# Performance work log

Measured on AMD Instinct MI355X. Metric: run time of the kernel, lower is better.

Reference implementation:

```python
import jax, jax.numpy as jnp
import numpy as np

B = 262144
FEATURES = 16
HID = 24
OUT = 784


def setup_inputs() -> dict:
    key = jax.random.key(0)
    ks = jax.random.split(key, 5)
    return {
        "x": jax.random.normal(ks[0], (B, FEATURES), dtype=jnp.float32),
        "W1": jax.random.normal(ks[1], (FEATURES, HID), dtype=jnp.float32) * 0.1,
        "b1": jax.random.normal(ks[2], (HID,), dtype=jnp.float32) * 0.1,
        "W2": jax.random.normal(ks[3], (HID, OUT), dtype=jnp.float32) * 0.1,
        "b2": jax.random.normal(ks[4], (OUT,), dtype=jnp.float32) * 0.1,
    }


def _relu_approx_sigmoid(x):
    # Original: relu(relu(x @ (0.25*I) + (ones-0.5)) @ (-I) + ones) @ (-I) + ones
    # x @ (0.25*I) == 0.25*x ; ones-0.5 == 0.5 ; y @ (-I) == -y.
    # => 1 - relu(1 - relu(0.25*x + 0.5))  (== clamp(0.25*x+0.5, 0, 1))
    a = jax.nn.relu(0.25 * x + 0.5)
    return 1.0 - jax.nn.relu(1.0 - a)


def reference(x, W1, b1, W2, b2):
    h = jax.nn.relu(x @ W1 + b1)          # [B, 24]
    return _relu_approx_sigmoid(h @ W2 + b2)  # [B, 784]
```

## Files before the change

### kernel.cpp

```cpp
#include <hip/hip_runtime.h>


typedef _Float16 f16x8 __attribute__((ext_vector_type(8)));
typedef float    f32x4 __attribute__((ext_vector_type(4)));
typedef unsigned int u32;

static __device__ __forceinline__ u32 pk_h2(float lo, float hi) {
    return __builtin_bit_cast(u32, __builtin_amdgcn_cvt_pkrtz(lo, hi));
}

#define THREADS 512
#define ROWS 256
#define F 16
#define H 24
#define NOUT 784
#define NCOLT 49
#define KP 12

__launch_bounds__(THREADS, 4)
__global__ void decoder_kernel(const float* __restrict__ x,
                               const float* __restrict__ W1,
                               const float* __restrict__ b1,
                               const float* __restrict__ W2,
                               const float* __restrict__ b2,
                               float* __restrict__ out) {
    __shared__ float w1t[H][F];
    __shared__ float b1s[H];
    __shared__ u32   hbuf[ROWS][16];
    __shared__ u32   w2b[NOUT][16];
    __shared__ float b2s[NOUT];

    const int tid  = threadIdx.x;
    const int row0 = blockIdx.x * ROWS;

    for (int idx = tid; idx < F * H; idx += THREADS) {
        const int i = idx / H, j = idx % H;
        w1t[j][i] = W1[idx];
    }
    if (tid < H) b1s[tid] = b1[tid];

    for (int c = tid; c < NOUT; c += THREADS)
        b2s[c] = fmaf(b2[c], 0.25f, 0.5f);

    for (int item = tid; item < NOUT * KP; item += THREADS) {
        const int col = item / KP, kp = item - col * KP;
        const float a = W2[(2 * kp + 0) * NOUT + col];
        const float c = W2[(2 * kp + 1) * NOUT + col];
        w2b[col][kp] = pk_h2(0.25f * a, 0.25f * c);
    }
    for (int item = tid; item < NOUT * 4; item += THREADS) {
        const int col = item >> 2, kp = 12 + (item & 3);
        w2b[col][kp] = 0u;
    }

    if (tid < ROWS) {
        float4 xv[4];
        const float* xr = x + (size_t)(row0 + tid) * F;
        #pragma unroll
        for (int q = 0; q < 4; ++q)
            xv[q] = *reinterpret_cast<const float4*>(&xr[q * 4]);

        #pragma unroll
        for (int g = 0; g < 3; ++g) {
            float hj[8];
            #pragma unroll
            for (int jj = 0; jj < 8; ++jj) {
                const int j = g * 8 + jj;
                float acc = b1s[j];
                #pragma unroll
                for (int q = 0; q < 4; ++q) {
                    const float4 wv = *reinterpret_cast<const float4*>(&w1t[j][q * 4]);
                    acc = fmaf(xv[q].x, wv.x, acc);
                    acc = fmaf(xv[q].y, wv.y, acc);
                    acc = fmaf(xv[q].z, wv.z, acc);
                    acc = fmaf(xv[q].w, wv.w, acc);
                }
                hj[jj] = fmaxf(acc, 0.0f);
            }
            uint4 p;
            p.x = pk_h2(hj[0], hj[1]);
            p.y = pk_h2(hj[2], hj[3]);
            p.z = pk_h2(hj[4], hj[5]);
            p.w = pk_h2(hj[6], hj[7]);
            *reinterpret_cast<uint4*>(&hbuf[tid][g * 4]) = p;
        }
        *reinterpret_cast<uint4*>(&hbuf[tid][12]) = make_uint4(0u, 0u, 0u, 0u);
    }

    __syncthreads();

    const int wave = tid >> 6;
    const int lane = tid & 63;
    const int lg   = lane >> 4;
    const int lm   = lane & 15;

    const f16x8 a0 = __builtin_bit_cast(f16x8,
        *reinterpret_cast<const uint4*>(&hbuf[wave * 32 + lm][lg * 4]));
    const f16x8 a1 = __builtin_bit_cast(f16x8,
        *reinterpret_cast<const uint4*>(&hbuf[wave * 32 + 16 + lm][lg * 4]));

    float* outp = out + ((size_t)row0 + wave * 32 + lg * 4) * NOUT + lm;

    for (int ct = 0; ct < NCOLT; ++ct) {
        const int cb = ct * 16;
        const f16x8 bf = __builtin_bit_cast(f16x8,
            *reinterpret_cast<const uint4*>(&w2b[cb + lm][lg * 4]));
        const float bb = b2s[cb + lm];
        f32x4 acc0 = {bb, bb, bb, bb};
        f32x4 acc1 = {bb, bb, bb, bb};
        acc0 = __builtin_amdgcn_mfma_f32_16x16x32_f16(a0, bf, acc0, 0, 0, 0);
        acc1 = __builtin_amdgcn_mfma_f32_16x16x32_f16(a1, bf, acc1, 0, 0, 0);

        float* p = outp + cb;
        #pragma unroll
        for (int r = 0; r < 4; ++r) {
            p[(size_t)r * NOUT]        = fminf(fmaxf(acc0[r], 0.f), 1.f);
            p[(size_t)(16 + r) * NOUT] = fminf(fmaxf(acc1[r], 0.f), 1.f);
        }
    }
}

extern "C" void kernel_launch(void* const* d_in, const int* in_sizes, int n_in,
                              void* d_out, int out_size, void* d_ws, size_t ws_size,
                              hipStream_t stream) {
    const float* x  = (const float*)d_in[0];
    const float* W1 = (const float*)d_in[1];
    const float* b1 = (const float*)d_in[2];
    const float* W2 = (const float*)d_in[3];
    const float* b2 = (const float*)d_in[4];
    float* out = (float*)d_out;

    const int B = in_sizes[0] / F;
    const int grid = B / ROWS;
    decoder_kernel<<<grid, THREADS, 0, stream>>>(x, W1, b1, W2, b2, out);
}
```

Baseline: 205.8 us.

## Transpose MFMA operands for float4 stores and swizzle W2 shared layout

Swaps the MFMA operand order so each lane's four accumulator values are consecutive output columns of a single row. The output can then be written with one float4 store per tile instead of four strided scalar stores. The packed W2 buffer in shared memory is XOR-swizzled to avoid LDS bank conflicts on the 16-byte reads, and the clamp uses fmed3. This aims to cut store instruction count and improve write coalescing on a store-bound kernel, at the cost of each wave's store footprint spanning 16 rows with 64-byte segments.

```diff
diff --git a/kernel.cpp b/kernel.cpp
--- a/kernel.cpp
+++ b/kernel.cpp
@@ -46,11 +46,11 @@
         const int col = item / KP, kp = item - col * KP;
         const float a = W2[(2 * kp + 0) * NOUT + col];
         const float c = W2[(2 * kp + 1) * NOUT + col];
-        w2b[col][kp] = pk_h2(0.25f * a, 0.25f * c);
+        w2b[col][kp ^ ((col & 3) << 2)] = pk_h2(0.25f * a, 0.25f * c);
     }
     for (int item = tid; item < NOUT * 4; item += THREADS) {
         const int col = item >> 2, kp = 12 + (item & 3);
-        w2b[col][kp] = 0u;
+        w2b[col][kp ^ ((col & 3) << 2)] = 0u;
     }
 
     if (tid < ROWS) {
@@ -94,29 +94,36 @@
     const int lg   = lane >> 4;
     const int lm   = lane & 15;
 
-    const f16x8 a0 = __builtin_bit_cast(f16x8,
+    const f16x8 hA = __builtin_bit_cast(f16x8,
         *reinterpret_cast<const uint4*>(&hbuf[wave * 32 + lm][lg * 4]));
-    const f16x8 a1 = __builtin_bit_cast(f16x8,
+    const f16x8 hB = __builtin_bit_cast(f16x8,
         *reinterpret_cast<const uint4*>(&hbuf[wave * 32 + 16 + lm][lg * 4]));
 
-    float* outp = out + ((size_t)row0 + wave * 32 + lg * 4) * NOUT + lm;
+    float* out0 = out + ((size_t)row0 + wave * 32 + lm) * NOUT + lg * 4;
+    float* out1 = out0 + (size_t)16 * NOUT;
+    const int wsw = (lg * 4) ^ ((lm & 3) << 2);
 
     for (int ct = 0; ct < NCOLT; ++ct) {
         const int cb = ct * 16;
-        const f16x8 bf = __builtin_bit_cast(f16x8,
-            *reinterpret_cast<const uint4*>(&w2b[cb + lm][lg * 4]));
-        const float bb = b2s[cb + lm];
-        f32x4 acc0 = {bb, bb, bb, bb};
-        f32x4 acc1 = {bb, bb, bb, bb};
-        acc0 = __builtin_amdgcn_mfma_f32_16x16x32_f16(a0, bf, acc0, 0, 0, 0);
-        acc1 = __builtin_amdgcn_mfma_f32_16x16x32_f16(a1, bf, acc1, 0, 0, 0);
+        const f16x8 wf = __builtin_bit_cast(f16x8,
+            *reinterpret_cast<const uint4*>(&w2b[cb + lm][wsw]));
+        const float4 bb = *reinterpret_cast<const float4*>(&b2s[cb + lg * 4]);
+        f32x4 acc0 = {bb.x, bb.y, bb.z, bb.w};
+        f32x4 acc1 = acc0;
+        acc0 = __builtin_amdgcn_mfma_f32_16x16x32_f16(wf, hA, acc0, 0, 0, 0);
+        acc1 = __builtin_amdgcn_mfma_f32_16x16x32_f16(wf, hB, acc1, 0, 0, 0);
 
-        float* p = outp + cb;
-        #pragma unroll
-        for (int r = 0; r < 4; ++r) {
-            p[(size_t)r * NOUT]        = fminf(fmaxf(acc0[r], 0.f), 1.f);
-            p[(size_t)(16 + r) * NOUT] = fminf(fmaxf(acc1[r], 0.f), 1.f);
-        }
+        float4 o0, o1;
+        o0.x = __builtin_amdgcn_fmed3f(acc0[0], 0.f, 1.f);
+        o0.y = __builtin_amdgcn_fmed3f(acc0[1], 0.f, 1.f);
+        o0.z = __builtin_amdgcn_fmed3f(acc0[2], 0.f, 1.f);
+        o0.w = __builtin_amdgcn_fmed3f(acc0[3], 0.f, 1.f);
+        o1.x = __builtin_amdgcn_fmed3f(acc1[0], 0.f, 1.f);
+        o1.y = __builtin_amdgcn_fmed3f(acc1[1], 0.f, 1.f);
+        o1.z = __builtin_amdgcn_fmed3f(acc1[2], 0.f, 1.f);
+        o1.w = __builtin_amdgcn_fmed3f(acc1[3], 0.f, 1.f);
+        *reinterpret_cast<float4*>(out0 + cb) = o0;
+        *reinterpret_cast<float4*>(out1 + cb) = o1;
     }
 }
 
```

Result: faster. 201.5 us (-2.1%).
